# Performance work log

Hardware: AMD Instinct MI355X
Metric: run time of the kernel (lower is better)

The kernel has to match this reference:

```python
import jax, jax.numpy as jnp
import numpy as np


def setup_inputs() -> dict:
    key = jax.random.key(0)
    k1, k2 = jax.random.split(key)
    H, D, N = 1, 256, 65536        # (heads=1, embedding_dim, num_tokens)
    C = 1024                       # num_embeddings (codebook size)
    inputs = jax.random.normal(k1, (H, D, N), dtype=jnp.float32)
    embedding = jax.random.normal(k2, (H, C, D), dtype=jnp.float32)
    return {"inputs": inputs, "embedding": embedding}


COMMITMENT_COST = 0.25


def reference(inputs, embedding):
    # inputs: (h, d, n) -> flat: (h, n, d)
    flat = jnp.transpose(inputs, (0, 2, 1))
    # negative euclidean distance (matches -torch.cdist, p=2)
    x2 = jnp.sum(flat * flat, axis=-1, keepdims=True)            # (h, n, 1)
    e2 = jnp.sum(embedding * embedding, axis=-1)[:, None, :]     # (h, 1, c)
    xe = jnp.einsum('hnd,hcd->hnc', flat, embedding)             # (h, n, c)
    d2 = jnp.maximum(x2 + e2 - 2.0 * xe, 0.0)
    distances = -jnp.sqrt(d2)                                    # (h, n, c)
    encoding_indices = jnp.argmax(distances, axis=2)             # (h, n)
    # gather codebook vectors: h == 1
    quantized = jnp.take(embedding[0], encoding_indices[0], axis=0)[None]  # (h, n, d)
    commit_loss = jnp.mean((jax.lax.stop_gradient(quantized) - flat) ** 2)
    loss = COMMITMENT_COST * commit_loss
    # straight-through estimator
    quantized_st = flat + jax.lax.stop_gradient(quantized - flat)
    out = jnp.transpose(quantized_st, (0, 2, 1))                 # (h, d, n)
    return out, encoding_indices, loss, distances
```

## Files before the change

### kernel.cpp

```cpp
#include <hip/hip_runtime.h>
#include <math.h>

#define N_TOK 65536
#define D_DIM 256
#define C_NUM 1024

#define OUT_OFF   0
#define IDX_OFF   (D_DIM * N_TOK)
#define LOSS_OFF  (IDX_OFF + N_TOK)
#define DIST_OFF  (LOSS_OFF + 1)

#define MARGIN 0.01f
#define NPART 4096

typedef __attribute__((ext_vector_type(8))) short bf16x8;
typedef __attribute__((ext_vector_type(4))) float f32x4;

static __device__ __forceinline__ unsigned short f2bf(float f) {
  unsigned int u = __float_as_uint(f);
  unsigned int r = (u + 0x7fffu + ((u >> 16) & 1u)) >> 16;
  return (unsigned short)r;
}
static __device__ __forceinline__ float bf2f(unsigned short h) {
  return __uint_as_float(((unsigned int)h) << 16);
}


#define WS_EH   0
#define WS_EL   524288
#define WS_E2   1048576
#define WS_PART 1052672
#define WS_TP   1069056
#define WS_NEEDED (WS_TP + (size_t)N_TOK * 16 * 8)

#define XH_OFF_F 0
#define XL_OFF_F 8388608

#define PART_OFF_F 263168

__global__ __launch_bounds__(256) void kA2_prep(const float* __restrict__ X,
                                                const float* __restrict__ E,
                                                float* __restrict__ out,
                                                unsigned char* __restrict__ ws) {
  const int bid = blockIdx.x, tid = threadIdx.x;
  if (bid < 1024) {
    unsigned short* XhG = (unsigned short*)(out + XH_OFF_F);
    unsigned short* XlG = (unsigned short*)(out + XL_OFF_F);
    const int n = bid * 64 + (tid >> 2);
    const int sg = (tid & 3) * 16;
    unsigned short* xh = XhG + (size_t)n * D_DIM;
    unsigned short* xl = XlG + (size_t)n * D_DIM;
#pragma unroll 1
    for (int dc = 0; dc < D_DIM; dc += 64) {
      float v[16];
#pragma unroll
      for (int j = 0; j < 16; ++j) v[j] = X[(size_t)(dc + sg + j) * N_TOK + n];
      unsigned short hh[16], ll[16];
#pragma unroll
      for (int j = 0; j < 16; ++j) {
        hh[j] = f2bf(v[j]);
        ll[j] = f2bf(v[j] - bf2f(hh[j]));
      }
      *(bf16x8*)(xh + dc + sg) = *(bf16x8*)&hh[0];
      *(bf16x8*)(xh + dc + sg + 8) = *(bf16x8*)&hh[8];
      *(bf16x8*)(xl + dc + sg) = *(bf16x8*)&ll[0];
      *(bf16x8*)(xl + dc + sg + 8) = *(bf16x8*)&ll[8];
    }
  } else if (bid < 1040) {
    unsigned short* EhG = (unsigned short*)(ws + WS_EH);
    unsigned short* ElG = (unsigned short*)(ws + WS_EL);
    float* e2p = (float*)(ws + WS_E2);
    const int lane = tid & 63, w = tid >> 6;
#pragma unroll 1
    for (int cc = 0; cc < 16; ++cc) {
      const int c = (bid - 1024) * 64 + w * 16 + cc;
      const float4 v = *(const float4*)(E + (size_t)c * D_DIM + lane * 4);
      unsigned short h0 = f2bf(v.x), h1 = f2bf(v.y), h2 = f2bf(v.z), h3 = f2bf(v.w);
      unsigned short l0 = f2bf(v.x - bf2f(h0)), l1 = f2bf(v.y - bf2f(h1));
      unsigned short l2 = f2bf(v.z - bf2f(h2)), l3 = f2bf(v.w - bf2f(h3));
      ushort4 hv = make_ushort4(h0, h1, h2, h3);
      ushort4 lv = make_ushort4(l0, l1, l2, l3);
      *(ushort4*)(EhG + (size_t)c * D_DIM + lane * 4) = hv;
      *(ushort4*)(ElG + (size_t)c * D_DIM + lane * 4) = lv;
      float s = v.x * v.x + v.y * v.y + v.z * v.z + v.w * v.w;
#pragma unroll
      for (int off = 32; off; off >>= 1) s += __shfl_down(s, off, 64);
      if (lane == 0) e2p[c] = s;
    }
  } else {
    const int n = (bid - 1040) * 256 + tid;
    float s = 0.0f;
#pragma unroll 8
    for (int d = 0; d < D_DIM; ++d) {
      float v = X[(size_t)d * N_TOK + n];
      s = fmaf(v, v, s);
    }
    out[IDX_OFF + n] = s;
  }
}

#define TM 64
#define TC 256
#define BK 32
#define XS2 264

__global__ __launch_bounds__(256) void k2c_dist(float* __restrict__ out,
                                                unsigned char* __restrict__ ws) {
  __shared__ __align__(16) unsigned short xh[TM * XS2];

  const unsigned short* __restrict__ XhG = (const unsigned short*)(out + XH_OFF_F);
  const unsigned short* __restrict__ XlG = (const unsigned short*)(out + XL_OFF_F);
  const unsigned short* __restrict__ EhG = (const unsigned short*)(ws + WS_EH);
  const float* __restrict__ e2p = (const float*)(ws + WS_E2);
  uint2* __restrict__ tp = (uint2*)(ws + WS_TP);

  const int tid = threadIdx.x;
  const int lane = tid & 63, wave = tid >> 6;

  const int bid = blockIdx.x;
  const int xcd = bid & 7;
  const int slot = bid >> 3;
  const int bx = slot & 3;
  const int by = xcd * 128 + (slot >> 2);
  const int c0 = bx * TC;
  const int n0 = by * TM;

  const int wc = c0 + wave * 64;
  const int m = lane & 15;
  const int q = lane >> 4;

  {
    const int tl = tid >> 2;
    const int seg = (tid & 3) * 64;
    const unsigned short* gh = XhG + (size_t)(n0 + tl) * D_DIM + seg;
    unsigned short* sh = xh + tl * XS2 + seg;
#pragma unroll
    for (int j = 0; j < 8; ++j)
      *(bf16x8*)(sh + j * 8) = *(const bf16x8*)(gh + j * 8);
  }
  __syncthreads();

  f32x4 acc[4][4];
#pragma unroll
  for (int i = 0; i < 4; ++i)
#pragma unroll
    for (int t = 0; t < 4; ++t) acc[i][t] = (f32x4){0.f, 0.f, 0.f, 0.f};

  const unsigned short* bp[4];
#pragma unroll
  for (int t = 0; t < 4; ++t) bp[t] = EhG + (size_t)(wc + t * 16 + m) * D_DIM + q * 8;
  const unsigned short* alp[4];
#pragma unroll
  for (int i = 0; i < 4; ++i) alp[i] = XlG + (size_t)(n0 + i * 16 + m) * D_DIM + q * 8;
  const size_t loEu = (size_t)(WS_EL - WS_EH) / 2;

#pragma unroll 2
  for (int kb = 0; kb < D_DIM; kb += BK) {
    bf16x8 ah[4], al[4], bh[4], bl[4];
#pragma unroll
    for (int t = 0; t < 4; ++t) {
      bh[t] = *(const bf16x8*)(bp[t] + kb);
      bl[t] = *(const bf16x8*)(bp[t] + loEu + kb);
    }
#pragma unroll
    for (int i = 0; i < 4; ++i) {
      const int ro = (i * 16 + m) * XS2 + kb + q * 8;
      ah[i] = *(const bf16x8*)&xh[ro];
      al[i] = *(const bf16x8*)(alp[i] + kb);
    }
#pragma unroll
    for (int i = 0; i < 4; ++i)
#pragma unroll
      for (int t = 0; t < 4; ++t) {
        acc[i][t] = __builtin_amdgcn_mfma_f32_16x16x32_bf16(ah[i], bh[t], acc[i][t], 0, 0, 0);
        acc[i][t] = __builtin_amdgcn_mfma_f32_16x16x32_bf16(ah[i], bl[t], acc[i][t], 0, 0, 0);
        acc[i][t] = __builtin_amdgcn_mfma_f32_16x16x32_bf16(al[i], bh[t], acc[i][t], 0, 0, 0);
      }
  }

  float e2v[4];
#pragma unroll
  for (int t = 0; t < 4; ++t) e2v[t] = e2p[wc + t * 16 + m];

#pragma unroll
  for (int i = 0; i < 4; ++i) {
#pragma unroll
    for (int r = 0; r < 4; ++r) {
      const int tok = n0 + i * 16 + q * 4 + r;
      const float x2v = out[IDX_OFF + tok];
      const size_t row = DIST_OFF + (size_t)tok * C_NUM;
      float dv[4];
      float bestv = -3.4e38f;
      int bidx = 0;
#pragma unroll
      for (int t = 0; t < 4; ++t) {
        float d2 = fmaf(-2.0f, acc[i][t][r], x2v + e2v[t]);
        d2 = fmaxf(d2, 0.0f);
        const float dd = -sqrtf(d2);
        dv[t] = dd;
        out[row + wc + t * 16 + m] = dd;
        if (dd > bestv) { bestv = dd; bidx = wc + t * 16 + m; }
      }
#pragma unroll
      for (int off = 1; off < 16; off <<= 1) {
        const float ov = __shfl_xor(bestv, off, 64);
        const int oi = __shfl_xor(bidx, off, 64);
        if (ov > bestv || (ov == bestv && oi < bidx)) { bestv = ov; bidx = oi; }
      }
      const float thr2 = bestv - MARGIN;
      int cnt = 0;
#pragma unroll
      for (int t = 0; t < 4; ++t) cnt += (dv[t] > thr2) ? 1 : 0;
#pragma unroll
      for (int off = 1; off < 16; off <<= 1) cnt += __shfl_xor(cnt, off, 64);
      if ((lane & 15) == 0) {
        tp[(size_t)tok * 16 + bx * 4 + wave] =
            make_uint2(__float_as_uint(bestv),
                       (unsigned)bidx | ((unsigned)cnt << 16));
      }
    }
  }
}

__global__ __launch_bounds__(256) void k3a2_argmax(const float* __restrict__ X,
                                                   const float* __restrict__ E,
                                                   float* __restrict__ out,
                                                   unsigned char* __restrict__ ws) {
  const uint2* __restrict__ tp = (const uint2*)(ws + WS_TP);
  float* __restrict__ part = (float*)(ws + WS_PART);
  __shared__ float lsum[4];
  const int tid = threadIdx.x, lane = tid & 63, w = tid >> 6;
  const int g = lane & 15, seg = lane >> 4;
  const int n = blockIdx.x * 16 + w * 4 + seg;

  const uint2 rec = tp[(size_t)n * 16 + g];
  const float val = __uint_as_float(rec.x);
  const int idx = (int)(rec.y & 0xffffu);
  const int cnt = (int)(rec.y >> 16);

  float best = val;
  int bi = idx, bc = cnt;
#pragma unroll
  for (int off = 1; off < 16; off <<= 1) {
    const float ov = __shfl_xor(best, off, 64);
    const int oi = __shfl_xor(bi, off, 64);
    const int oc = __shfl_xor(bc, off, 64);
    if (ov > best || (ov == best && oi < bi)) { best = ov; bi = oi; bc = oc; }
  }
  const float thr = best - MARGIN;
  const unsigned long long bal = __ballot(val > thr);
  const int m16 = (int)((bal >> (seg * 16)) & 0xffffull);
  const bool fast = (__popc((unsigned)m16) == 1) && (bc == 1);

  float lval = 0.0f;
  if (fast && g == 0) {
    out[IDX_OFF + n] = (float)bi;
    lval = best * best;
  }

  unsigned long long smask = __ballot((!fast) && (g == 0));
  float sloss = 0.0f;
  while (smask) {
    const int sl = __ffsll((long long)smask) - 1;
    smask &= smask - 1;
    const int nn = blockIdx.x * 16 + w * 4 + (sl >> 4);
    {
      const float* row = out + DIST_OFF + (size_t)nn * C_NUM;
      float v[16];
      float bestf = -3.4e38f;
      int bif = 0x7fffffff;
#pragma unroll
      for (int j = 0; j < 16; ++j) {
        v[j] = row[j * 64 + lane];
        if (v[j] > bestf) { bestf = v[j]; bif = j * 64 + lane; }
      }
#pragma unroll
      for (int off = 32; off; off >>= 1) {
        const float ov = __shfl_xor(bestf, off, 64);
        const int oi = __shfl_xor(bif, off, 64);
        if (ov > bestf || (ov == bestf && oi < bif)) { bestf = ov; bif = oi; }
      }
      const float thrf = bestf - MARGIN;
      unsigned long long masks[16];
      int total = 0;
#pragma unroll
      for (int j = 0; j < 16; ++j) {
        masks[j] = __ballot(v[j] > thrf);
        total += __popcll(masks[j]);
      }
      float best_d2 = bestf * bestf;
      int best_idx = bif;
      if (total > 1) {
        best_d2 = 3.4e38f;
        best_idx = 0x7fffffff;
        for (int j = 0; j < 16; ++j) {
          unsigned long long mm = masks[j];
          while (mm) {
            const int l = __ffsll((long long)mm) - 1;
            mm &= mm - 1;
            const int c = j * 64 + l;
            float sx = 0.f, se = 0.f, sxe = 0.f;
#pragma unroll
            for (int r = 0; r < 4; ++r) {
              const int d = r * 64 + lane;
              const float xv = X[(size_t)d * N_TOK + nn];
              const float ev = E[(size_t)c * D_DIM + d];
              sx = fmaf(xv, xv, sx);
              se = fmaf(ev, ev, se);
              sxe = fmaf(xv, ev, sxe);
            }
            float d2 = fmaf(-2.f, sxe, sx + se);
#pragma unroll
            for (int off = 32; off; off >>= 1) d2 += __shfl_xor(d2, off, 64);
            d2 = fmaxf(d2, 0.f);
            if (d2 < best_d2 || (d2 == best_d2 && c < best_idx)) {
              best_d2 = d2; best_idx = c;
            }
          }
        }
      }
      if (lane == 0) {
        out[IDX_OFF + nn] = (float)best_idx;
        sloss += best_d2;
      }
    }
  }

  float wl = lval + ((lane == 0) ? sloss : 0.0f);
#pragma unroll
  for (int off = 32; off; off >>= 1) wl += __shfl_down(wl, off, 64);
  if (lane == 0) lsum[w] = wl;
  __syncthreads();
  if (tid == 0)
    part[blockIdx.x] = lsum[0] + lsum[1] + lsum[2] + lsum[3];
}

__global__ __launch_bounds__(256) void k3b2_loss(float* __restrict__ out,
                                                 unsigned char* __restrict__ ws) {
  const float* __restrict__ part = (const float*)(ws + WS_PART);
  __shared__ float red[4];
  const int tid = threadIdx.x, lane = tid & 63, w = tid >> 6;
  float s = 0.0f;
#pragma unroll
  for (int i = 0; i < NPART / 256; ++i) s += part[i * 256 + tid];
#pragma unroll
  for (int off = 32; off; off >>= 1) s += __shfl_down(s, off, 64);
  if (lane == 0) red[w] = s;
  __syncthreads();
  if (tid == 0)
    out[LOSS_OFF] = (red[0] + red[1] + red[2] + red[3]) *
                    (0.25f / ((float)N_TOK * (float)D_DIM));
}

#define EH_OFF_F  0
#define EL_OFF_F  131072
#define E2_OFF_F  262144

__global__ __launch_bounds__(256) void kA_prep(const float* __restrict__ X,
                                               const float* __restrict__ E,
                                               float* __restrict__ out) {
  const int bid = blockIdx.x, tid = threadIdx.x;
  if (bid < 256) {
    const int n = bid * 256 + tid;
    float s = 0.0f;
#pragma unroll 8
    for (int d = 0; d < D_DIM; ++d) {
      float v = X[(size_t)d * N_TOK + n];
      s = fmaf(v, v, s);
    }
    out[IDX_OFF + n] = s;
  } else {
    unsigned short* EhG = (unsigned short*)(out + EH_OFF_F);
    unsigned short* ElG = (unsigned short*)(out + EL_OFF_F);
    const int lane = tid & 63, w = tid >> 6;
#pragma unroll 1
    for (int cc = 0; cc < 16; ++cc) {
      const int c = (bid - 256) * 64 + w * 16 + cc;
      const float4 v = *(const float4*)(E + (size_t)c * D_DIM + lane * 4);
      unsigned short h0 = f2bf(v.x), h1 = f2bf(v.y), h2 = f2bf(v.z), h3 = f2bf(v.w);
      unsigned short l0 = f2bf(v.x - bf2f(h0)), l1 = f2bf(v.y - bf2f(h1));
      unsigned short l2 = f2bf(v.z - bf2f(h2)), l3 = f2bf(v.w - bf2f(h3));
      ushort4 hv = make_ushort4(h0, h1, h2, h3);
      ushort4 lv = make_ushort4(l0, l1, l2, l3);
      *(ushort4*)(EhG + (size_t)c * D_DIM + lane * 4) = hv;
      *(ushort4*)(ElG + (size_t)c * D_DIM + lane * 4) = lv;
      float s = v.x * v.x + v.y * v.y + v.z * v.z + v.w * v.w;
#pragma unroll
      for (int off = 32; off; off >>= 1) s += __shfl_down(s, off, 64);
      if (lane == 0) out[E2_OFF_F + c] = s;
    }
  }
}

#define XS 40

__global__ __launch_bounds__(256) void k2_dist(const float* __restrict__ X,
                                               float* __restrict__ out) {
  __shared__ __align__(16) unsigned short xhb[2][TM * XS];
  __shared__ __align__(16) unsigned short xlb[2][TM * XS];

  const unsigned short* __restrict__ EhG = (const unsigned short*)(out + EH_OFF_F);
  const unsigned short* __restrict__ ElG = (const unsigned short*)(out + EL_OFF_F);

  const int tid = threadIdx.x;
  const int lane = tid & 63, wave = tid >> 6;
  const int bid = blockIdx.x;
  const int xcd = bid & 7;
  const int slot = bid >> 3;
  const int bx = slot & 3;
  const int by = xcd * 128 + (slot >> 2);
  const int c0 = bx * TC;
  const int n0 = by * TM;

  const int wc = c0 + wave * 64;
  const int m = lane & 15;
  const int q = lane >> 4;

  f32x4 acc[4][4];
#pragma unroll
  for (int i = 0; i < 4; ++i)
#pragma unroll
    for (int t = 0; t < 4; ++t) acc[i][t] = (f32x4){0.f, 0.f, 0.f, 0.f};

  const int sn = lane;
  const int kg = wave;

  float xv[8];
  {
    const float* xp = X + (size_t)(kg * 8) * N_TOK + n0 + sn;
#pragma unroll
    for (int j = 0; j < 8; ++j) xv[j] = xp[(size_t)j * N_TOK];
  }

#pragma unroll 1
  for (int kb = 0; kb < D_DIM; kb += BK) {
    const int p = (kb >> 5) & 1;
    bf16x8 bh[4], bl[4];
#pragma unroll
    for (int t = 0; t < 4; ++t) {
      const size_t eoff = (size_t)(wc + t * 16 + m) * D_DIM + kb + q * 8;
      bh[t] = *(const bf16x8*)(EhG + eoff);
      bl[t] = *(const bf16x8*)(ElG + eoff);
    }
    unsigned short hh[8], ll[8];
#pragma unroll
    for (int j = 0; j < 8; ++j) {
      hh[j] = f2bf(xv[j]);
      ll[j] = f2bf(xv[j] - bf2f(hh[j]));
    }
    *(bf16x8*)&xhb[p][sn * XS + kg * 8] = *(bf16x8*)hh;
    *(bf16x8*)&xlb[p][sn * XS + kg * 8] = *(bf16x8*)ll;
    if (kb + BK < D_DIM) {
      const float* xp = X + (size_t)(kb + BK + kg * 8) * N_TOK + n0 + sn;
#pragma unroll
      for (int j = 0; j < 8; ++j) xv[j] = xp[(size_t)j * N_TOK];
    }
    __syncthreads();
    bf16x8 ah[4], al[4];
#pragma unroll
    for (int i = 0; i < 4; ++i) {
      const int ro = (i * 16 + m) * XS + q * 8;
      ah[i] = *(const bf16x8*)&xhb[p][ro];
      al[i] = *(const bf16x8*)&xlb[p][ro];
    }
#pragma unroll
    for (int i = 0; i < 4; ++i)
#pragma unroll
      for (int t = 0; t < 4; ++t) {
        acc[i][t] = __builtin_amdgcn_mfma_f32_16x16x32_bf16(ah[i], bh[t], acc[i][t], 0, 0, 0);
        acc[i][t] = __builtin_amdgcn_mfma_f32_16x16x32_bf16(ah[i], bl[t], acc[i][t], 0, 0, 0);
        acc[i][t] = __builtin_amdgcn_mfma_f32_16x16x32_bf16(al[i], bh[t], acc[i][t], 0, 0, 0);
      }
  }

  float e2v[4];
#pragma unroll
  for (int t = 0; t < 4; ++t) e2v[t] = out[E2_OFF_F + wc + t * 16 + m];

#pragma unroll
  for (int i = 0; i < 4; ++i) {
#pragma unroll
    for (int r = 0; r < 4; ++r) {
      const int tok = n0 + i * 16 + q * 4 + r;
      const float x2v = out[IDX_OFF + tok];
      const size_t row = DIST_OFF + (size_t)tok * C_NUM;
#pragma unroll
      for (int t = 0; t < 4; ++t) {
        float d2 = fmaf(-2.0f, acc[i][t][r], x2v + e2v[t]);
        d2 = fmaxf(d2, 0.0f);
        out[row + wc + t * 16 + m] = -sqrtf(d2);
      }
    }
  }
}

__global__ __launch_bounds__(256) void k3_argmax(const float* __restrict__ X,
                                                 const float* __restrict__ E,
                                                 float* __restrict__ out) {
  __shared__ float lsum[4];
  const int tid = threadIdx.x, lane = tid & 63, w = tid >> 6;
  float wloss = 0.0f;

#pragma unroll 1
  for (int it = 0; it < 4; ++it) {
    const int n = blockIdx.x * 16 + w * 4 + it;
    const float* row = out + DIST_OFF + (size_t)n * C_NUM;

    float v[16];
    float best = -3.4e38f;
    int bi = 0x7fffffff;
#pragma unroll
    for (int j = 0; j < 16; ++j) {
      v[j] = row[j * 64 + lane];
      if (v[j] > best) { best = v[j]; bi = j * 64 + lane; }
    }
#pragma unroll
    for (int off = 32; off; off >>= 1) {
      const float ov = __shfl_xor(best, off, 64);
      const int oi = __shfl_xor(bi, off, 64);
      if (ov > best || (ov == best && oi < bi)) { best = ov; bi = oi; }
    }
    const float thr = best - MARGIN;
    unsigned long long masks[16];
    int total = 0;
#pragma unroll
    for (int j = 0; j < 16; ++j) {
      masks[j] = __ballot(v[j] > thr);
      total += __popcll(masks[j]);
    }
    float best_d2 = best * best;
    int best_idx = bi;
    if (total > 1) {
      best_d2 = 3.4e38f;
      best_idx = 0x7fffffff;
      for (int j = 0; j < 16; ++j) {
        unsigned long long mm = masks[j];
        while (mm) {
          const int l = __ffsll((long long)mm) - 1;
          mm &= mm - 1;
          const int c = j * 64 + l;
          float sx = 0.f, se = 0.f, sxe = 0.f;
#pragma unroll
          for (int r = 0; r < 4; ++r) {
            const int d = r * 64 + lane;
            const float xv = X[(size_t)d * N_TOK + n];
            const float ev = E[(size_t)c * D_DIM + d];
            sx = fmaf(xv, xv, sx);
            se = fmaf(ev, ev, se);
            sxe = fmaf(xv, ev, sxe);
          }
          float d2 = fmaf(-2.f, sxe, sx + se);
#pragma unroll
          for (int off = 32; off; off >>= 1) d2 += __shfl_xor(d2, off, 64);
          d2 = fmaxf(d2, 0.f);
          if (d2 < best_d2 || (d2 == best_d2 && c < best_idx)) {
            best_d2 = d2; best_idx = c;
          }
        }
      }
    }
    if (lane == 0) out[IDX_OFF + n] = (float)best_idx;
    wloss += best_d2;
  }
  if (lane == 0) lsum[w] = wloss;
  __syncthreads();
  if (tid == 0)
    out[PART_OFF_F + blockIdx.x] = lsum[0] + lsum[1] + lsum[2] + lsum[3];
}

__global__ __launch_bounds__(256) void k3b_loss(float* __restrict__ out) {
  __shared__ float red[4];
  const int tid = threadIdx.x, lane = tid & 63, w = tid >> 6;
  float s = 0.0f;
#pragma unroll
  for (int i = 0; i < NPART / 256; ++i) s += out[PART_OFF_F + i * 256 + tid];
#pragma unroll
  for (int off = 32; off; off >>= 1) s += __shfl_down(s, off, 64);
  if (lane == 0) red[w] = s;
  __syncthreads();
  if (tid == 0)
    out[LOSS_OFF] = (red[0] + red[1] + red[2] + red[3]) *
                    (0.25f / ((float)N_TOK * (float)D_DIM));
}

__global__ __launch_bounds__(256) void k4_gather(const float* __restrict__ E,
                                                 float* __restrict__ out) {
  const int g = blockIdx.x * 256 + threadIdx.x;
  const int n = g * 4;
  const int i0 = (int)out[IDX_OFF + n + 0];
  const int i1 = (int)out[IDX_OFF + n + 1];
  const int i2 = (int)out[IDX_OFF + n + 2];
  const int i3 = (int)out[IDX_OFF + n + 3];
  const float* e0 = E + (size_t)i0 * D_DIM;
  const float* e1 = E + (size_t)i1 * D_DIM;
  const float* e2 = E + (size_t)i2 * D_DIM;
  const float* e3 = E + (size_t)i3 * D_DIM;
  const int d0 = blockIdx.y * 32;
#pragma unroll 4
  for (int d = d0; d < d0 + 32; ++d) {
    float4 wv = make_float4(e0[d], e1[d], e2[d], e3[d]);
    *(float4*)&out[(size_t)d * N_TOK + n] = wv;
  }
}

extern "C" void kernel_launch(void* const* d_in, const int* in_sizes, int n_in,
                              void* d_out, int out_size, void* d_ws, size_t ws_size,
                              hipStream_t stream) {
  const float* X = (const float*)d_in[0];
  const float* E = (const float*)d_in[1];
  float* out = (float*)d_out;

  if (ws_size >= WS_NEEDED && d_ws != nullptr) {
    unsigned char* ws = (unsigned char*)d_ws;
    hipLaunchKernelGGL(kA2_prep, dim3(1296), dim3(256), 0, stream, X, E, out, ws);
    hipLaunchKernelGGL(k2c_dist, dim3((C_NUM / TC) * (N_TOK / TM)), dim3(256), 0,
                       stream, out, ws);
    hipLaunchKernelGGL(k3a2_argmax, dim3(N_TOK / 16), dim3(256), 0, stream,
                       X, E, out, ws);
    hipLaunchKernelGGL(k3b2_loss, dim3(1), dim3(256), 0, stream, out, ws);
    hipLaunchKernelGGL(k4_gather, dim3(N_TOK / 4 / 256, 8), dim3(256), 0, stream,
                       E, out);
  } else {
    hipLaunchKernelGGL(kA_prep, dim3(272), dim3(256), 0, stream, X, E, out);
    hipLaunchKernelGGL(k2_dist, dim3((C_NUM / TC) * (N_TOK / TM)), dim3(256), 0,
                       stream, X, out);
    hipLaunchKernelGGL(k3_argmax, dim3(N_TOK / 16), dim3(256), 0, stream, X, E, out);
    hipLaunchKernelGGL(k3b_loss, dim3(1), dim3(256), 0, stream, out);
    hipLaunchKernelGGL(k4_gather, dim3(N_TOK / 4 / 256, 8), dim3(256), 0, stream,
                       E, out);
  }
}
```

Measured before the change: 701.0 us.

## Fuse x2 into prep, stage Xl in LDS, simplify dist epilogue argmax records

The squared token norms are now computed inside the bf16 split pass, which removes a separate strided reread of X by extra blocks. The low-part X tile is staged in shared memory alongside the high part, so the MFMA loop no longer reads it from global memory. The distance epilogue now writes only a per-group max value, dropping index and count tracking. The argmax kernel instead rereads one 64-wide slice of the distance row to recover the index and count, trading epilogue ALU and shuffle work for an extra global read. Shared memory per block doubles, which may lower occupancy.

```diff
diff --git a/kernel.cpp b/kernel.cpp
--- a/kernel.cpp
+++ b/kernel.cpp
@@ -31,7 +31,7 @@
 #define WS_E2   1048576
 #define WS_PART 1052672
 #define WS_TP   1069056
-#define WS_NEEDED (WS_TP + (size_t)N_TOK * 16 * 8)
+#define WS_NEEDED (WS_TP + (size_t)N_TOK * 16 * 4)
 
 #define XH_OFF_F 0
 #define XL_OFF_F 8388608
@@ -50,6 +50,7 @@
     const int sg = (tid & 3) * 16;
     unsigned short* xh = XhG + (size_t)n * D_DIM;
     unsigned short* xl = XlG + (size_t)n * D_DIM;
+    float s = 0.0f;
 #pragma unroll 1
     for (int dc = 0; dc < D_DIM; dc += 64) {
       float v[16];
@@ -58,6 +59,7 @@
       unsigned short hh[16], ll[16];
 #pragma unroll
       for (int j = 0; j < 16; ++j) {
+        s = fmaf(v[j], v[j], s);
         hh[j] = f2bf(v[j]);
         ll[j] = f2bf(v[j] - bf2f(hh[j]));
       }
@@ -66,7 +68,10 @@
       *(bf16x8*)(xl + dc + sg) = *(bf16x8*)&ll[0];
       *(bf16x8*)(xl + dc + sg + 8) = *(bf16x8*)&ll[8];
     }
-  } else if (bid < 1040) {
+    s += __shfl_xor(s, 1, 64);
+    s += __shfl_xor(s, 2, 64);
+    if ((tid & 3) == 0) out[IDX_OFF + n] = s;
+  } else {
     unsigned short* EhG = (unsigned short*)(ws + WS_EH);
     unsigned short* ElG = (unsigned short*)(ws + WS_EL);
     float* e2p = (float*)(ws + WS_E2);
@@ -87,15 +92,6 @@
       for (int off = 32; off; off >>= 1) s += __shfl_down(s, off, 64);
       if (lane == 0) e2p[c] = s;
     }
-  } else {
-    const int n = (bid - 1040) * 256 + tid;
-    float s = 0.0f;
-#pragma unroll 8
-    for (int d = 0; d < D_DIM; ++d) {
-      float v = X[(size_t)d * N_TOK + n];
-      s = fmaf(v, v, s);
-    }
-    out[IDX_OFF + n] = s;
   }
 }
 
@@ -107,12 +103,13 @@
 __global__ __launch_bounds__(256) void k2c_dist(float* __restrict__ out,
                                                 unsigned char* __restrict__ ws) {
   __shared__ __align__(16) unsigned short xh[TM * XS2];
+  __shared__ __align__(16) unsigned short xl[TM * XS2];
 
   const unsigned short* __restrict__ XhG = (const unsigned short*)(out + XH_OFF_F);
   const unsigned short* __restrict__ XlG = (const unsigned short*)(out + XL_OFF_F);
   const unsigned short* __restrict__ EhG = (const unsigned short*)(ws + WS_EH);
   const float* __restrict__ e2p = (const float*)(ws + WS_E2);
-  uint2* __restrict__ tp = (uint2*)(ws + WS_TP);
+  float* __restrict__ tpv = (float*)(ws + WS_TP);
 
   const int tid = threadIdx.x;
   const int lane = tid & 63, wave = tid >> 6;
@@ -133,11 +130,26 @@
     const int tl = tid >> 2;
     const int seg = (tid & 3) * 64;
     const unsigned short* gh = XhG + (size_t)(n0 + tl) * D_DIM + seg;
+    const unsigned short* gl = XlG + (size_t)(n0 + tl) * D_DIM + seg;
     unsigned short* sh = xh + tl * XS2 + seg;
-#pragma unroll
-    for (int j = 0; j < 8; ++j)
+    unsigned short* sl = xl + tl * XS2 + seg;
+#pragma unroll
+    for (int j = 0; j < 8; ++j) {
       *(bf16x8*)(sh + j * 8) = *(const bf16x8*)(gh + j * 8);
-  }
+      *(bf16x8*)(sl + j * 8) = *(const bf16x8*)(gl + j * 8);
+    }
+  }
+
+  float x2r[16];
+#pragma unroll
+  for (int i = 0; i < 4; ++i)
+#pragma unroll
+    for (int r = 0; r < 4; ++r)
+      x2r[i * 4 + r] = out[IDX_OFF + n0 + i * 16 + q * 4 + r];
+  float e2v[4];
+#pragma unroll
+  for (int t = 0; t < 4; ++t) e2v[t] = e2p[wc + t * 16 + m];
+
   __syncthreads();
 
   f32x4 acc[4][4];
@@ -149,9 +161,6 @@
   const unsigned short* bp[4];
 #pragma unroll
   for (int t = 0; t < 4; ++t) bp[t] = EhG + (size_t)(wc + t * 16 + m) * D_DIM + q * 8;
-  const unsigned short* alp[4];
-#pragma unroll
-  for (int i = 0; i < 4; ++i) alp[i] = XlG + (size_t)(n0 + i * 16 + m) * D_DIM + q * 8;
   const size_t loEu = (size_t)(WS_EL - WS_EH) / 2;
 
 #pragma unroll 2
@@ -166,7 +175,7 @@
     for (int i = 0; i < 4; ++i) {
       const int ro = (i * 16 + m) * XS2 + kb + q * 8;
       ah[i] = *(const bf16x8*)&xh[ro];
-      al[i] = *(const bf16x8*)(alp[i] + kb);
+      al[i] = *(const bf16x8*)&xl[ro];
     }
 #pragma unroll
     for (int i = 0; i < 4; ++i)
@@ -178,84 +187,76 @@
       }
   }
 
-  float e2v[4];
-#pragma unroll
-  for (int t = 0; t < 4; ++t) e2v[t] = e2p[wc + t * 16 + m];
-
 #pragma unroll
   for (int i = 0; i < 4; ++i) {
 #pragma unroll
     for (int r = 0; r < 4; ++r) {
       const int tok = n0 + i * 16 + q * 4 + r;
-      const float x2v = out[IDX_OFF + tok];
+      const float x2v = x2r[i * 4 + r];
       const size_t row = DIST_OFF + (size_t)tok * C_NUM;
-      float dv[4];
       float bestv = -3.4e38f;
-      int bidx = 0;
 #pragma unroll
       for (int t = 0; t < 4; ++t) {
         float d2 = fmaf(-2.0f, acc[i][t][r], x2v + e2v[t]);
         d2 = fmaxf(d2, 0.0f);
         const float dd = -sqrtf(d2);
-        dv[t] = dd;
         out[row + wc + t * 16 + m] = dd;
-        if (dd > bestv) { bestv = dd; bidx = wc + t * 16 + m; }
-      }
-#pragma unroll
-      for (int off = 1; off < 16; off <<= 1) {
-        const float ov = __shfl_xor(bestv, off, 64);
-        const int oi = __shfl_xor(bidx, off, 64);
-        if (ov > bestv || (ov == bestv && oi < bidx)) { bestv = ov; bidx = oi; }
-      }
-      const float thr2 = bestv - MARGIN;
-      int cnt = 0;
-#pragma unroll
-      for (int t = 0; t < 4; ++t) cnt += (dv[t] > thr2) ? 1 : 0;
-#pragma unroll
-      for (int off = 1; off < 16; off <<= 1) cnt += __shfl_xor(cnt, off, 64);
-      if ((lane & 15) == 0) {
-        tp[(size_t)tok * 16 + bx * 4 + wave] =
-            make_uint2(__float_as_uint(bestv),
-                       (unsigned)bidx | ((unsigned)cnt << 16));
-      }
-    }
-  }
-}
-
-__global__ __launch_bounds__(256) void k3a2_argmax(const float* __restrict__ X,
+        bestv = fmaxf(bestv, dd);
+      }
+#pragma unroll
+      for (int off = 1; off < 16; off <<= 1)
+        bestv = fmaxf(bestv, __shfl_xor(bestv, off, 64));
+      if ((lane & 15) == 0)
+        tpv[(size_t)tok * 16 + bx * 4 + wave] = bestv;
+    }
+  }
+}
+
+__global__ __launch_bounds__(256) void k3a4_argmax(const float* __restrict__ X,
                                                    const float* __restrict__ E,
                                                    float* __restrict__ out,
                                                    unsigned char* __restrict__ ws) {
-  const uint2* __restrict__ tp = (const uint2*)(ws + WS_TP);
+  const float* __restrict__ tpv = (const float*)(ws + WS_TP);
   float* __restrict__ part = (float*)(ws + WS_PART);
   __shared__ float lsum[4];
   const int tid = threadIdx.x, lane = tid & 63, w = tid >> 6;
   const int g = lane & 15, seg = lane >> 4;
   const int n = blockIdx.x * 16 + w * 4 + seg;
 
-  const uint2 rec = tp[(size_t)n * 16 + g];
-  const float val = __uint_as_float(rec.x);
-  const int idx = (int)(rec.y & 0xffffu);
-  const int cnt = (int)(rec.y >> 16);
-
-  float best = val;
-  int bi = idx, bc = cnt;
+  const float gval = tpv[(size_t)n * 16 + g];
+  float best = gval;
+#pragma unroll
+  for (int off = 1; off < 16; off <<= 1)
+    best = fmaxf(best, __shfl_xor(best, off, 64));
+  const float thr = best - MARGIN;
+  const unsigned long long bal = __ballot(gval > thr);
+  const unsigned m16 = (unsigned)((bal >> (seg * 16)) & 0xffffull);
+  const int nflag = __popc(m16);
+  const int j = __ffs(m16) - 1;
+
+  const float4 rv =
+      *(const float4*)(out + DIST_OFF + (size_t)n * C_NUM + j * 64 + g * 4);
+
+  float bv = rv.x;
+  int bix = j * 64 + g * 4;
+  if (rv.y > bv) { bv = rv.y; bix = j * 64 + g * 4 + 1; }
+  if (rv.z > bv) { bv = rv.z; bix = j * 64 + g * 4 + 2; }
+  if (rv.w > bv) { bv = rv.w; bix = j * 64 + g * 4 + 3; }
+  int cnt = (rv.x > thr ? 1 : 0) + (rv.y > thr ? 1 : 0) +
+            (rv.z > thr ? 1 : 0) + (rv.w > thr ? 1 : 0);
 #pragma unroll
   for (int off = 1; off < 16; off <<= 1) {
-    const float ov = __shfl_xor(best, off, 64);
-    const int oi = __shfl_xor(bi, off, 64);
-    const int oc = __shfl_xor(bc, off, 64);
-    if (ov > best || (ov == best && oi < bi)) { best = ov; bi = oi; bc = oc; }
-  }
-  const float thr = best - MARGIN;
-  const unsigned long long bal = __ballot(val > thr);
-  const int m16 = (int)((bal >> (seg * 16)) & 0xffffull);
-  const bool fast = (__popc((unsigned)m16) == 1) && (bc == 1);
-
+    const float ov = __shfl_xor(bv, off, 64);
+    const int oi = __shfl_xor(bix, off, 64);
+    cnt += __shfl_xor(cnt, off, 64);
+    if (ov > bv || (ov == bv && oi < bix)) { bv = ov; bix = oi; }
+  }
+
+  const bool fast = (nflag == 1) && (cnt == 1);
   float lval = 0.0f;
   if (fast && g == 0) {
-    out[IDX_OFF + n] = (float)bi;
-    lval = best * best;
+    out[IDX_OFF + n] = (float)bix;
+    lval = bv * bv;
   }
 
   unsigned long long smask = __ballot((!fast) && (g == 0));
@@ -270,9 +271,9 @@
       float bestf = -3.4e38f;
       int bif = 0x7fffffff;
 #pragma unroll
-      for (int j = 0; j < 16; ++j) {
-        v[j] = row[j * 64 + lane];
-        if (v[j] > bestf) { bestf = v[j]; bif = j * 64 + lane; }
+      for (int jj = 0; jj < 16; ++jj) {
+        v[jj] = row[jj * 64 + lane];
+        if (v[jj] > bestf) { bestf = v[jj]; bif = jj * 64 + lane; }
       }
 #pragma unroll
       for (int off = 32; off; off >>= 1) {
@@ -284,21 +285,21 @@
       unsigned long long masks[16];
       int total = 0;
 #pragma unroll
-      for (int j = 0; j < 16; ++j) {
-        masks[j] = __ballot(v[j] > thrf);
-        total += __popcll(masks[j]);
+      for (int jj = 0; jj < 16; ++jj) {
+        masks[jj] = __ballot(v[jj] > thrf);
+        total += __popcll(masks[jj]);
       }
       float best_d2 = bestf * bestf;
       int best_idx = bif;
       if (total > 1) {
         best_d2 = 3.4e38f;
         best_idx = 0x7fffffff;
-        for (int j = 0; j < 16; ++j) {
-          unsigned long long mm = masks[j];
+        for (int jj = 0; jj < 16; ++jj) {
+          unsigned long long mm = masks[jj];
           while (mm) {
             const int l = __ffsll((long long)mm) - 1;
             mm &= mm - 1;
-            const int c = j * 64 + l;
+            const int c = jj * 64 + l;
             float sx = 0.f, se = 0.f, sxe = 0.f;
 #pragma unroll
             for (int r = 0; r < 4; ++r) {
@@ -587,10 +588,11 @@
                                                  float* __restrict__ out) {
   const int g = blockIdx.x * 256 + threadIdx.x;
   const int n = g * 4;
-  const int i0 = (int)out[IDX_OFF + n + 0];
-  const int i1 = (int)out[IDX_OFF + n + 1];
-  const int i2 = (int)out[IDX_OFF + n + 2];
-  const int i3 = (int)out[IDX_OFF + n + 3];
+  const float4 iv = *(const float4*)&out[IDX_OFF + n];
+  const int i0 = (int)iv.x;
+  const int i1 = (int)iv.y;
+  const int i2 = (int)iv.z;
+  const int i3 = (int)iv.w;
   const float* e0 = E + (size_t)i0 * D_DIM;
   const float* e1 = E + (size_t)i1 * D_DIM;
   const float* e2 = E + (size_t)i2 * D_DIM;
@@ -612,10 +614,10 @@
 
   if (ws_size >= WS_NEEDED && d_ws != nullptr) {
     unsigned char* ws = (unsigned char*)d_ws;
-    hipLaunchKernelGGL(kA2_prep, dim3(1296), dim3(256), 0, stream, X, E, out, ws);
+    hipLaunchKernelGGL(kA2_prep, dim3(1040), dim3(256), 0, stream, X, E, out, ws);
     hipLaunchKernelGGL(k2c_dist, dim3((C_NUM / TC) * (N_TOK / TM)), dim3(256), 0,
                        stream, out, ws);
-    hipLaunchKernelGGL(k3a2_argmax, dim3(N_TOK / 16), dim3(256), 0, stream,
+    hipLaunchKernelGGL(k3a4_argmax, dim3(N_TOK / 16), dim3(256), 0, stream,
                        X, E, out, ws);
     hipLaunchKernelGGL(k3b2_loss, dim3(1), dim3(256), 0, stream, out, ws);
     hipLaunchKernelGGL(k4_gather, dim3(N_TOK / 4 / 256, 8), dim3(256), 0, stream,
```

Result: faster. 614.4 us (-12.4%).
